# Performance work log

Hardware: AMD Instinct MI355X
Metric: run time of the kernel (lower is better)

## Reference

```python
import jax, jax.numpy as jnp
import numpy as np

NEG_INF = -1e30  # stand-in for -inf that is safe under fp16/bf16 softmax


def setup_inputs() -> dict:
    key = jax.random.key(0)
    k1, k2, k3, k4 = jax.random.split(key, 4)
    B, S, D_IN, D_OUT = 4, 4096, 2048, 2048
    x = jax.random.normal(k1, (B, S, D_IN), dtype=jnp.float32)
    scale = 0.02
    Wq = jax.random.normal(k2, (D_IN, D_OUT), dtype=jnp.float32) * scale
    Wk = jax.random.normal(k3, (D_IN, D_OUT), dtype=jnp.float32) * scale
    Wv = jax.random.normal(k4, (D_IN, D_OUT), dtype=jnp.float32) * scale
    return {"x": x, "Wq": Wq, "Wk": Wk, "Wv": Wv}


def reference(x, Wq, Wk, Wv):
    # x: [B, S, d_in]; Wq/Wk/Wv: [d_in, d_out] (torch Linear weight transposed)
    B, S, _ = x.shape
    q = jnp.einsum('bsd,de->bse', x, Wq)
    k = jnp.einsum('bsd,de->bse', x, Wk)
    v = jnp.einsum('bsd,de->bse', x, Wv)
    d_k = k.shape[-1]
    scale = 1.0 / jnp.sqrt(jnp.asarray(d_k, dtype=x.dtype))
    # attn_scores[b, i, j] = q_i . k_j
    scores = jnp.einsum('bqe,bke->bqk', q, k) * scale
    # causal mask: position i attends to j <= i
    i = jnp.arange(S)[:, None]
    j = jnp.arange(S)[None, :]
    scores = jnp.where(j > i, NEG_INF, scores)
    attn = jax.nn.softmax(scores, axis=-1)
    # dropout p=0.0 / eval mode -> identity
    return jnp.einsum('bqk,bke->bqe', attn, v)
```

## Files before the change

kernel.cpp:

```cpp
#include <hip/hip_runtime.h>

using u16   = unsigned short;
using s16x8 = __attribute__((ext_vector_type(8))) short;
using u16x8 = __attribute__((ext_vector_type(8))) unsigned short;
using f32x4 = __attribute__((ext_vector_type(4))) float;

__device__ __forceinline__ u16 f2bf(float f) {
    unsigned u = __float_as_uint(f);
    u += 0x7FFFu + ((u >> 16) & 1u);
    return (u16)(u >> 16);
}

__device__ __forceinline__ void gload16(const void* g, void* l) {
    __builtin_amdgcn_global_load_lds((const __attribute__((address_space(1))) void*)g,
                                     (__attribute__((address_space(3))) void*)l, 16, 0, 0);
}

#define MFMA_BF16(a, b, d) \
    d = __builtin_amdgcn_mfma_f32_16x16x32_bf16(a, b, d, 0, 0, 0)

__device__ __forceinline__ void gemm256_core(
    const u16* __restrict__ A, const u16* __restrict__ Bt,
    int lda, int ldb, int kSteps, u16* lds, f32x4 (&acc)[8][4])
{
    const int tid  = threadIdx.x;
    const int lane = tid & 63;
    const int wid  = tid >> 6;
    const int wr   = wid >> 2;
    const int wc   = wid & 3;
    const int c    = lane & 15;
    const int g    = lane >> 4;

    const int srow = tid >> 3;
    const int scol = ((tid & 7) * 8) ^ ((srow & 7) << 3);
    const u16* pA = A  + (size_t)srow * lda + scol;
    const u16* pB = Bt + (size_t)srow * ldb + scol;
    const size_t sA = (size_t)64 * lda;
    const size_t sB = (size_t)64 * ldb;
    const int ldst = tid * 8;

    const int low0 = (g * 8)      ^ ((c & 7) << 3);
    const int low1 = (32 + g * 8) ^ ((c & 7) << 3);
    const int aRow = (wr * 128 + c) * 64;
    const int bRow = (wc * 64 + c) * 64;

    {
        u16* wA = lds;
        u16* wB = lds + 16384;
        gload16(pA + 0 * sA, wA + 0 * 4096 + ldst);
        gload16(pA + 2 * sA, wA + 2 * 4096 + ldst);
        gload16(pB + 0 * sB, wB + 0 * 4096 + ldst);
        gload16(pB + 1 * sB, wB + 1 * 4096 + ldst);
        gload16(pB + 2 * sB, wB + 2 * 4096 + ldst);
        gload16(pB + 3 * sB, wB + 3 * 4096 + ldst);
        gload16(pA + 1 * sA, wA + 1 * 4096 + ldst);
        gload16(pA + 3 * sA, wA + 3 * 4096 + ldst);
    }
    if (kSteps > 1) { pA += 64; pB += 64; }

    for (int t = 0; t < kSteps; ++t) {
        const u16* rdA = lds + (t & 1) * 32768;
        const u16* rdB = rdA + 16384;
        u16* wA = lds + ((t & 1) ^ 1) * 32768;
        u16* wB = wA + 16384;
        const bool more = (t + 1 < kSteps);

        s16x8 av[4][2], bv[2][2], bw[2][2];

        asm volatile("s_waitcnt vmcnt(2)" ::: "memory");
        __builtin_amdgcn_s_barrier();
        __builtin_amdgcn_sched_barrier(0);
        if (more) {
            gload16(pA + 0 * sA, wA + 0 * 4096 + ldst);
            gload16(pA + 2 * sA, wA + 2 * 4096 + ldst);
            gload16(pB + 0 * sB, wB + 0 * 4096 + ldst);
            gload16(pB + 1 * sB, wB + 1 * 4096 + ldst);
            gload16(pB + 2 * sB, wB + 2 * 4096 + ldst);
            gload16(pB + 3 * sB, wB + 3 * 4096 + ldst);
        }
#pragma unroll
        for (int m = 0; m < 4; ++m) {
            av[m][0] = *(const s16x8*)(rdA + aRow + m * 1024 + low0);
            av[m][1] = *(const s16x8*)(rdA + aRow + m * 1024 + low1);
        }
#pragma unroll
        for (int n = 0; n < 2; ++n) {
            bv[n][0] = *(const s16x8*)(rdB + bRow + n * 1024 + low0);
            bv[n][1] = *(const s16x8*)(rdB + bRow + n * 1024 + low1);
        }
        __builtin_amdgcn_s_setprio(1);
#pragma unroll
        for (int m = 0; m < 4; ++m)
#pragma unroll
            for (int n = 0; n < 2; ++n) {
                MFMA_BF16(av[m][0], bv[n][0], acc[m][n]);
                MFMA_BF16(av[m][1], bv[n][1], acc[m][n]);
            }
        __builtin_amdgcn_s_setprio(0);
        __builtin_amdgcn_s_barrier();

#pragma unroll
        for (int n = 0; n < 2; ++n) {
            bw[n][0] = *(const s16x8*)(rdB + bRow + (n + 2) * 1024 + low0);
            bw[n][1] = *(const s16x8*)(rdB + bRow + (n + 2) * 1024 + low1);
        }
        if (more) {
            gload16(pA + 1 * sA, wA + 1 * 4096 + ldst);
            gload16(pA + 3 * sA, wA + 3 * 4096 + ldst);
        }
        __builtin_amdgcn_s_setprio(1);
#pragma unroll
        for (int m = 0; m < 4; ++m)
#pragma unroll
            for (int n = 0; n < 2; ++n) {
                MFMA_BF16(av[m][0], bw[n][0], acc[m][n + 2]);
                MFMA_BF16(av[m][1], bw[n][1], acc[m][n + 2]);
            }
        __builtin_amdgcn_s_setprio(0);

        if (more) asm volatile("s_waitcnt vmcnt(8)" ::: "memory");
        else      asm volatile("s_waitcnt vmcnt(0)" ::: "memory");
        __builtin_amdgcn_s_barrier();
        __builtin_amdgcn_sched_barrier(0);
#pragma unroll
        for (int m = 0; m < 4; ++m) {
            av[m][0] = *(const s16x8*)(rdA + aRow + (m + 4) * 1024 + low0);
            av[m][1] = *(const s16x8*)(rdA + aRow + (m + 4) * 1024 + low1);
        }
        __builtin_amdgcn_s_setprio(1);
#pragma unroll
        for (int m = 0; m < 4; ++m)
#pragma unroll
            for (int n = 0; n < 2; ++n) {
                MFMA_BF16(av[m][0], bw[n][0], acc[m + 4][n + 2]);
                MFMA_BF16(av[m][1], bw[n][1], acc[m + 4][n + 2]);
            }
        __builtin_amdgcn_s_setprio(0);
        __builtin_amdgcn_s_barrier();

        __builtin_amdgcn_s_setprio(1);
#pragma unroll
        for (int m = 0; m < 4; ++m)
#pragma unroll
            for (int n = 0; n < 2; ++n) {
                MFMA_BF16(av[m][0], bv[n][0], acc[m + 4][n]);
                MFMA_BF16(av[m][1], bv[n][1], acc[m + 4][n]);
            }
        __builtin_amdgcn_s_setprio(0);

        if (t + 2 < kSteps) { pA += 64; pB += 64; }
    }
    asm volatile("s_waitcnt vmcnt(0)" ::: "memory");
}

__device__ __forceinline__ int xcd_swz(int bid, int nwg) {
    return (bid & 7) * (nwg >> 3) + (bid >> 3);
}

__global__ __launch_bounds__(512, 2) void gemm256_bf16(
    const u16* __restrict__ A, const u16* __restrict__ Bt, u16* __restrict__ C,
    int N, int K, long aBatch, long bBatch, long cBatch)
{
    __shared__ u16 lds[65536];
    const int bid = xcd_swz((int)blockIdx.x, (int)gridDim.x);
    const int nT = N >> 8;
    const int m0 = (bid / nT) << 8;
    const int n0 = (bid % nT) << 8;
    const int b  = blockIdx.z;
    const u16* Ab = A  + (size_t)b * aBatch + (size_t)m0 * K;
    const u16* Bb = Bt + (size_t)b * bBatch + (size_t)n0 * K;
    f32x4 acc[8][4] = {};
    gemm256_core(Ab, Bb, K, K, K >> 6, lds, acc);

    u16* Cb = C + (size_t)b * cBatch;
    const int lane = threadIdx.x & 63;
    const int c = lane & 15, g = lane >> 4;
    const int wid = threadIdx.x >> 6;
    const int rowb = m0 + (wid >> 2) * 128 + g * 4;
    const int colb = n0 + (wid & 3) * 64 + c;
#pragma unroll
    for (int m = 0; m < 8; ++m)
#pragma unroll
        for (int n = 0; n < 4; ++n)
#pragma unroll
            for (int r = 0; r < 4; ++r)
                Cb[(size_t)(rowb + m * 16 + r) * N + colb + n * 16] = f2bf(acc[m][n][r]);
}

__global__ __launch_bounds__(512, 2) void attn_score256(
    const u16* __restrict__ Tm, const u16* __restrict__ Xb,
    u16* __restrict__ P, float* __restrict__ L, long pStride, int bBase)
{
    __shared__ u16 lds[65536];
    const int b  = bBase + blockIdx.z;
    const int wg = xcd_swz((int)blockIdx.x, (int)gridDim.x);
    int it = (int)((sqrtf(8.0f * (float)wg + 1.0f) - 1.0f) * 0.5f);
    while ((it + 1) * (it + 2) / 2 <= wg) ++it;
    while (it * (it + 1) / 2 > wg) --it;
    const int jt = wg - it * (it + 1) / 2;
    const int i0 = it << 8, j0 = jt << 8;

    const u16* Ab = Tm + ((size_t)b * 4096 + i0) * 2048;
    const u16* Bb = Xb + ((size_t)b * 4096 + j0) * 2048;
    f32x4 acc[8][4] = {};
    gemm256_core(Ab, Bb, 2048, 2048, 32, lds, acc);

    u16*   Pb = P + (size_t)blockIdx.z * pStride;
    float* Lb = L + (size_t)b * 4096;
    const int lane = threadIdx.x & 63;
    const int c = lane & 15, g = lane >> 4;
    const int wid = threadIdx.x >> 6;
    const int rowb = i0 + (wid >> 2) * 128 + g * 4;
    const int colb = j0 + (wid & 3) * 64 + c;
    const float SCALE = 0.022097086912079608f;

    float rsum[8][4];
#pragma unroll
    for (int m = 0; m < 8; ++m)
#pragma unroll
        for (int r = 0; r < 4; ++r) rsum[m][r] = 0.0f;
#pragma unroll
    for (int m = 0; m < 8; ++m) {
#pragma unroll
        for (int r = 0; r < 4; ++r) {
            const int Ig = rowb + m * 16 + r;
#pragma unroll
            for (int n = 0; n < 4; ++n) {
                const int Jg = colb + n * 16;
                float p = (Jg > Ig) ? 0.0f : __expf(acc[m][n][r] * SCALE);
                Pb[(size_t)Ig * 4096 + Jg] = f2bf(p);
                rsum[m][r] += p;
            }
        }
    }
#pragma unroll
    for (int m = 0; m < 8; ++m)
#pragma unroll
        for (int r = 0; r < 4; ++r) {
            float v = rsum[m][r];
            v += __shfl_xor(v, 1);
            v += __shfl_xor(v, 2);
            v += __shfl_xor(v, 4);
            v += __shfl_xor(v, 8);
            rsum[m][r] = v;
        }
    if (c == 0) {
#pragma unroll
        for (int m = 0; m < 8; ++m)
#pragma unroll
            for (int r = 0; r < 4; ++r)
                atomicAdd(&Lb[rowb + m * 16 + r], rsum[m][r]);
    }
}

__global__ __launch_bounds__(512, 2) void attn_pv256(
    const u16* __restrict__ P, const u16* __restrict__ Vt,
    const float* __restrict__ L, float* __restrict__ Out,
    long pStride, int bBase, int zCount)
{
    __shared__ u16 lds[65536];
    const int d = (int)blockIdx.x;
    const int x = d & 7;
    const int q = d >> 3;
    const int spr = zCount << 3;
    const int s = q % spr;
    const int r = q / spr;
    const int nt = s & 7;
    const int z  = s >> 3;
    const int it = r ? x : 15 - x;
    const int b  = bBase + z;
    const int i0 = it << 8, n0 = nt << 8;

    const u16* Ab = P  + (size_t)z * pStride + (size_t)i0 * 4096;
    const u16* Bb = Vt + (size_t)b * (2048ll * 4096) + (size_t)n0 * 4096;
    f32x4 acc[8][4] = {};
    gemm256_core(Ab, Bb, 4096, 4096, (it + 1) * 4, lds, acc);

    const float* Lb = L + (size_t)b * 4096;
    float* Ob = Out + (size_t)b * (4096ll * 2048);
    const int lane = threadIdx.x & 63;
    const int c = lane & 15, g = lane >> 4;
    const int wid = threadIdx.x >> 6;
    const int rowb = i0 + (wid >> 2) * 128 + g * 4;
    const int colb = n0 + (wid & 3) * 64 + c;
#pragma unroll
    for (int m = 0; m < 8; ++m) {
#pragma unroll
        for (int r2 = 0; r2 < 4; ++r2) {
            const int I = rowb + m * 16 + r2;
            const float inv = 1.0f / Lb[I];
#pragma unroll
            for (int n = 0; n < 4; ++n)
                Ob[(size_t)I * 2048 + colb + n * 16] = acc[m][n][r2] * inv;
        }
    }
}

__device__ __forceinline__ void gemm_core_128(
    const u16* __restrict__ A, const u16* __restrict__ Bt,
    int lda, int ldb, int kSteps,
    u16* ldsA, u16* ldsB, f32x4 (&acc)[4][4])
{
    const int tid  = threadIdx.x;
    const int lane = tid & 63;
    const int wr   = (tid >> 7) & 1;
    const int wc   = (tid >> 6) & 1;
    const int g    = lane >> 4;
    const int c    = lane & 15;

    const u16* aSrc = A  + (size_t)(tid >> 3) * lda + (tid & 7) * 8;
    const u16* bSrc = Bt + (size_t)(tid >> 3) * ldb + (tid & 7) * 8;
    u16* aDst = ldsA + tid * 8;
    u16* bDst = ldsB + tid * 8;

    for (int kt = 0; kt < kSteps; ++kt) {
#pragma unroll
        for (int it = 0; it < 4; ++it) {
            gload16(aSrc + (size_t)it * 32 * lda, aDst + it * 2048);
            gload16(bSrc + (size_t)it * 32 * ldb, bDst + it * 2048);
        }
        aSrc += 64; bSrc += 64;
        __syncthreads();
#pragma unroll
        for (int kk = 0; kk < 2; ++kk) {
            s16x8 av[4], bv[4];
#pragma unroll
            for (int m = 0; m < 4; ++m)
                av[m] = *(const s16x8*)(ldsA + (size_t)(wr*64 + m*16 + c) * 64 + kk*32 + g*8);
#pragma unroll
            for (int n = 0; n < 4; ++n)
                bv[n] = *(const s16x8*)(ldsB + (size_t)(wc*64 + n*16 + c) * 64 + kk*32 + g*8);
#pragma unroll
            for (int m = 0; m < 4; ++m)
#pragma unroll
                for (int n = 0; n < 4; ++n)
                    MFMA_BF16(av[m], bv[n], acc[m][n]);
        }
        __syncthreads();
    }
}

__global__ __launch_bounds__(256) void gemm_bt_bf16(
    const u16* __restrict__ A, const u16* __restrict__ Bt, u16* __restrict__ C,
    int N, int K)
{
    __shared__ u16 ldsA[128 * 64];
    __shared__ u16 ldsB[128 * 64];
    const int nT = N >> 7;
    const int m0 = (int)(blockIdx.x / nT) << 7;
    const int n0 = (int)(blockIdx.x % nT) << 7;
    const u16* Ab = A + (size_t)m0 * K;
    const u16* Bb = Bt + (size_t)n0 * K;
    f32x4 acc[4][4] = {};
    gemm_core_128(Ab, Bb, K, K, K >> 6, ldsA, ldsB, acc);

    const int lane = threadIdx.x & 63;
    const int wr = (threadIdx.x >> 7) & 1, wc = (threadIdx.x >> 6) & 1;
    const int rb = m0 + wr * 64 + ((lane >> 4) << 2);
    const int cb = n0 + wc * 64 + (lane & 15);
#pragma unroll
    for (int m = 0; m < 4; ++m)
#pragma unroll
        for (int n = 0; n < 4; ++n)
#pragma unroll
            for (int r = 0; r < 4; ++r)
                C[(size_t)(rb + m*16 + r) * N + cb + n*16] = f2bf(acc[m][n][r]);
}

__global__ __launch_bounds__(256) void cvt_f32_bf16x8(
    const float* __restrict__ in, u16* __restrict__ out, long n8)
{
    long i = (long)blockIdx.x * 256 + threadIdx.x;
    if (i >= n8) return;
    const float4* p = (const float4*)(in + i * 8);
    float4 v0 = p[0], v1 = p[1];
    u16x8 o;
    o[0] = f2bf(v0.x); o[1] = f2bf(v0.y); o[2] = f2bf(v0.z); o[3] = f2bf(v0.w);
    o[4] = f2bf(v1.x); o[5] = f2bf(v1.y); o[6] = f2bf(v1.z); o[7] = f2bf(v1.w);
    *(u16x8*)(out + i * 8) = o;
}

__global__ __launch_bounds__(256) void transpose_cvt(
    const float* __restrict__ W, u16* __restrict__ Wt, int dim)
{
    __shared__ float tile[64][65];
    const int nb = dim >> 6;
    const int br = blockIdx.x / nb, bc = blockIdx.x % nb;
    const int t  = threadIdx.x;
    const int lr = t >> 2;
    const int lc = (t & 3) << 4;
    const float* src = W + (size_t)(br * 64 + lr) * dim + bc * 64 + lc;
#pragma unroll
    for (int q = 0; q < 4; ++q) {
        float4 v = *(const float4*)(src + q * 4);
        tile[lr][lc + q * 4 + 0] = v.x;
        tile[lr][lc + q * 4 + 1] = v.y;
        tile[lr][lc + q * 4 + 2] = v.z;
        tile[lr][lc + q * 4 + 3] = v.w;
    }
    __syncthreads();
    u16* dst = Wt + (size_t)(bc * 64 + lr) * dim + br * 64 + lc;
    u16x8 o0, o1;
#pragma unroll
    for (int q = 0; q < 8; ++q) o0[q] = f2bf(tile[lc + q][lr]);
#pragma unroll
    for (int q = 0; q < 8; ++q) o1[q] = f2bf(tile[lc + 8 + q][lr]);
    *(u16x8*)(dst)     = o0;
    *(u16x8*)(dst + 8) = o1;
}

__global__ __launch_bounds__(256) void zero_f32(float* p, int n)
{
    int i = blockIdx.x * 256 + threadIdx.x;
    if (i < n) p[i] = 0.0f;
}

extern "C" void kernel_launch(void* const* d_in, const int* in_sizes, int n_in,
                              void* d_out, int out_size, void* d_ws, size_t ws_size,
                              hipStream_t stream)
{
    const float* x  = (const float*)d_in[0];
    const float* Wq = (const float*)d_in[1];
    const float* Wk = (const float*)d_in[2];
    const float* Wv = (const float*)d_in[3];
    float* out = (float*)d_out;

    char* ws = (char*)d_ws;
    u16*   xb  = (u16*)(ws + 0ull);
    u16*   Tm  = (u16*)(ws + 67108864ull);
    u16*   Vt  = (u16*)(ws + 134217728ull);
    u16*   Wqb = (u16*)(ws + 201326592ull);
    u16*   Wkb = (u16*)(ws + 209715200ull);
    u16*   Wvt = (u16*)(ws + 218103808ull);
    u16*   Mt  = (u16*)(ws + 226492416ull);
    float* L   = (float*)(ws + 234881024ull);
    u16*   P   = (u16*)(ws + 234946560ull);
    const size_t needBase = 234946560ull;
    const size_t needFull = needBase + 134217728ull;
    const size_t needPerB = needBase + 33554432ull;
    if (ws_size < needPerB) return;

    cvt_f32_bf16x8<<<16384, 256, 0, stream>>>(x,  xb,  4194304);
    cvt_f32_bf16x8<<<2048,  256, 0, stream>>>(Wq, Wqb, 524288);
    cvt_f32_bf16x8<<<2048,  256, 0, stream>>>(Wk, Wkb, 524288);
    transpose_cvt <<<1024,  256, 0, stream>>>(Wv, Wvt, 2048);

    gemm_bt_bf16<<<dim3(256, 1, 1), 256, 0, stream>>>(Wkb, Wqb, Mt, 2048, 2048);
    gemm256_bf16<<<dim3(512, 1, 1), 512, 0, stream>>>(xb, Mt, Tm, 2048, 2048, 0, 0, 0);
    gemm256_bf16<<<dim3(128, 1, 4), 512, 0, stream>>>(Wvt, xb, Vt, 4096, 2048,
                                                      0, 8388608, 8388608);
    zero_f32<<<64, 256, 0, stream>>>(L, 16384);

    if (ws_size >= needFull) {
        attn_score256<<<dim3(136, 1, 4), 512, 0, stream>>>(Tm, xb, P, L, 16777216ll, 0);
        attn_pv256   <<<dim3(512, 1, 1), 512, 0, stream>>>(P, Vt, L, out, 16777216ll, 0, 4);
    } else {
        for (int b = 0; b < 4; ++b) {
            attn_score256<<<dim3(136, 1, 1), 512, 0, stream>>>(Tm, xb, P, L, 0, b);
            attn_pv256   <<<dim3(128, 1, 1), 512, 0, stream>>>(P, Vt, L, out, 0, b, 1);
        }
    }
}
```

Measured before the change: 640.9 us.

## Restructure GEMM double-buffer pipeline with two-stage prologue and whole-tile staging

Restructures the bf16 GEMM main loop. The prologue now preloads the first two K-steps into both LDS buffers. Each later iteration issues all eight global-to-LDS loads for a future step at once, instead of splitting them into groups of six and two. A separate register set for the second A half is added, along with extra barriers and lgkmcnt waits around each MFMA phase, so that LDS reads finish before compute starts. The goal is deeper prefetch and better overlap of memory and MFMA work, at the cost of more barriers per iteration and higher register pressure.

```diff
diff --git a/kernel.cpp b/kernel.cpp
--- a/kernel.cpp
+++ b/kernel.cpp
@@ -33,8 +33,8 @@
 
     const int srow = tid >> 3;
     const int scol = ((tid & 7) * 8) ^ ((srow & 7) << 3);
-    const u16* pA = A  + (size_t)srow * lda + scol;
-    const u16* pB = Bt + (size_t)srow * ldb + scol;
+    const u16* pA0 = A  + (size_t)srow * lda + scol;
+    const u16* pB0 = Bt + (size_t)srow * ldb + scol;
     const size_t sA = (size_t)64 * lda;
     const size_t sB = (size_t)64 * ldb;
     const int ldst = tid * 8;
@@ -44,40 +44,39 @@
     const int aRow = (wr * 128 + c) * 64;
     const int bRow = (wc * 64 + c) * 64;
 
-    {
-        u16* wA = lds;
-        u16* wB = lds + 16384;
-        gload16(pA + 0 * sA, wA + 0 * 4096 + ldst);
-        gload16(pA + 2 * sA, wA + 2 * 4096 + ldst);
-        gload16(pB + 0 * sB, wB + 0 * 4096 + ldst);
-        gload16(pB + 1 * sB, wB + 1 * 4096 + ldst);
-        gload16(pB + 2 * sB, wB + 2 * 4096 + ldst);
-        gload16(pB + 3 * sB, wB + 3 * 4096 + ldst);
-        gload16(pA + 1 * sA, wA + 1 * 4096 + ldst);
-        gload16(pA + 3 * sA, wA + 3 * 4096 + ldst);
-    }
-    if (kSteps > 1) { pA += 64; pB += 64; }
+#define STAGE8(buf, qa, qb)                                    \
+    do {                                                       \
+        u16* wA_ = (buf);                                      \
+        u16* wB_ = (buf) + 16384;                              \
+        gload16((qa) + 0 * sA, wA_ + 0 * 4096 + ldst);         \
+        gload16((qa) + 2 * sA, wA_ + 2 * 4096 + ldst);         \
+        gload16((qb) + 0 * sB, wB_ + 0 * 4096 + ldst);         \
+        gload16((qb) + 1 * sB, wB_ + 1 * 4096 + ldst);         \
+        gload16((qb) + 2 * sB, wB_ + 2 * 4096 + ldst);         \
+        gload16((qb) + 3 * sB, wB_ + 3 * 4096 + ldst);         \
+        gload16((qa) + 1 * sA, wA_ + 1 * 4096 + ldst);         \
+        gload16((qa) + 3 * sA, wA_ + 3 * 4096 + ldst);         \
+    } while (0)
+
+    STAGE8(lds, pA0, pB0);
+    if (kSteps > 1) STAGE8(lds + 32768, pA0 + 64, pB0 + 64);
+    const u16* pA = pA0 + 128;
+    const u16* pB = pB0 + 128;
+
+    if (kSteps > 1) asm volatile("s_waitcnt vmcnt(10)" ::: "memory");
+    else            asm volatile("s_waitcnt vmcnt(2)"  ::: "memory");
+    __builtin_amdgcn_s_barrier();
 
     for (int t = 0; t < kSteps; ++t) {
         const u16* rdA = lds + (t & 1) * 32768;
         const u16* rdB = rdA + 16384;
-        u16* wA = lds + ((t & 1) ^ 1) * 32768;
-        u16* wB = wA + 16384;
-        const bool more = (t + 1 < kSteps);
-
-        s16x8 av[4][2], bv[2][2], bw[2][2];
-
-        asm volatile("s_waitcnt vmcnt(2)" ::: "memory");
-        __builtin_amdgcn_s_barrier();
-        __builtin_amdgcn_sched_barrier(0);
-        if (more) {
-            gload16(pA + 0 * sA, wA + 0 * 4096 + ldst);
-            gload16(pA + 2 * sA, wA + 2 * 4096 + ldst);
-            gload16(pB + 0 * sB, wB + 0 * 4096 + ldst);
-            gload16(pB + 1 * sB, wB + 1 * 4096 + ldst);
-            gload16(pB + 2 * sB, wB + 2 * 4096 + ldst);
-            gload16(pB + 3 * sB, wB + 3 * 4096 + ldst);
-        }
+        u16* wbuf = lds + ((t & 1) ^ 1) * 32768;
+        const bool doStage = (t >= 1) && (t + 1 < kSteps);
+        const bool last = (t + 1 == kSteps);
+
+        s16x8 av[4][2], aw[4][2], bv[2][2], bw[2][2];
+
+        if (doStage) { STAGE8(wbuf, pA, pB); pA += 64; pB += 64; }
 #pragma unroll
         for (int m = 0; m < 4; ++m) {
             av[m][0] = *(const s16x8*)(rdA + aRow + m * 1024 + low0);
@@ -88,6 +87,9 @@
             bv[n][0] = *(const s16x8*)(rdB + bRow + n * 1024 + low0);
             bv[n][1] = *(const s16x8*)(rdB + bRow + n * 1024 + low1);
         }
+        __builtin_amdgcn_s_barrier();
+        asm volatile("s_waitcnt lgkmcnt(0)" ::: "memory");
+        __builtin_amdgcn_sched_barrier(0);
         __builtin_amdgcn_s_setprio(1);
 #pragma unroll
         for (int m = 0; m < 4; ++m)
@@ -104,10 +106,9 @@
             bw[n][0] = *(const s16x8*)(rdB + bRow + (n + 2) * 1024 + low0);
             bw[n][1] = *(const s16x8*)(rdB + bRow + (n + 2) * 1024 + low1);
         }
-        if (more) {
-            gload16(pA + 1 * sA, wA + 1 * 4096 + ldst);
-            gload16(pA + 3 * sA, wA + 3 * 4096 + ldst);
-        }
+        __builtin_amdgcn_s_barrier();
+        asm volatile("s_waitcnt lgkmcnt(0)" ::: "memory");
+        __builtin_amdgcn_sched_barrier(0);
         __builtin_amdgcn_s_setprio(1);
 #pragma unroll
         for (int m = 0; m < 4; ++m)
@@ -117,23 +118,25 @@
                 MFMA_BF16(av[m][1], bw[n][1], acc[m][n + 2]);
             }
         __builtin_amdgcn_s_setprio(0);
-
-        if (more) asm volatile("s_waitcnt vmcnt(8)" ::: "memory");
-        else      asm volatile("s_waitcnt vmcnt(0)" ::: "memory");
-        __builtin_amdgcn_s_barrier();
+        if (last) asm volatile("s_waitcnt vmcnt(0)" ::: "memory");
+        else      asm volatile("s_waitcnt vmcnt(8)" ::: "memory");
+        __builtin_amdgcn_s_barrier();
+
+#pragma unroll
+        for (int m = 0; m < 4; ++m) {
+            aw[m][0] = *(const s16x8*)(rdA + aRow + (m + 4) * 1024 + low0);
+            aw[m][1] = *(const s16x8*)(rdA + aRow + (m + 4) * 1024 + low1);
+        }
+        __builtin_amdgcn_s_barrier();
+        asm volatile("s_waitcnt lgkmcnt(0)" ::: "memory");
         __builtin_amdgcn_sched_barrier(0);
-#pragma unroll
-        for (int m = 0; m < 4; ++m) {
-            av[m][0] = *(const s16x8*)(rdA + aRow + (m + 4) * 1024 + low0);
-            av[m][1] = *(const s16x8*)(rdA + aRow + (m + 4) * 1024 + low1);
-        }
         __builtin_amdgcn_s_setprio(1);
 #pragma unroll
         for (int m = 0; m < 4; ++m)
 #pragma unroll
             for (int n = 0; n < 2; ++n) {
-                MFMA_BF16(av[m][0], bw[n][0], acc[m + 4][n + 2]);
-                MFMA_BF16(av[m][1], bw[n][1], acc[m + 4][n + 2]);
+                MFMA_BF16(aw[m][0], bw[n][0], acc[m + 4][n + 2]);
+                MFMA_BF16(aw[m][1], bw[n][1], acc[m + 4][n + 2]);
             }
         __builtin_amdgcn_s_setprio(0);
         __builtin_amdgcn_s_barrier();
@@ -143,14 +146,14 @@
         for (int m = 0; m < 4; ++m)
 #pragma unroll
             for (int n = 0; n < 2; ++n) {
-                MFMA_BF16(av[m][0], bv[n][0], acc[m + 4][n]);
-                MFMA_BF16(av[m][1], bv[n][1], acc[m + 4][n]);
+                MFMA_BF16(aw[m][0], bv[n][0], acc[m + 4][n]);
+                MFMA_BF16(aw[m][1], bv[n][1], acc[m + 4][n]);
             }
         __builtin_amdgcn_s_setprio(0);
-
-        if (t + 2 < kSteps) { pA += 64; pB += 64; }
-    }
-    asm volatile("s_waitcnt vmcnt(0)" ::: "memory");
+        if (!last) asm volatile("s_waitcnt vmcnt(2)" ::: "memory");
+        __builtin_amdgcn_s_barrier();
+    }
+#undef STAGE8
 }
 
 __device__ __forceinline__ int xcd_swz(int bid, int nwg) {
```

After: 716.1 us. 11.7% more time.
